# Performance work log

Hardware: AMD Instinct MI355X
Metric: run time of the kernel (lower is better)

Reference implementation:

```python
import jax, jax.numpy as jnp
import numpy as np


def setup_inputs() -> dict:
    key = jax.random.key(0)
    k1, k2, k3 = jax.random.split(key, 3)
    B, C, H, W = 8, 256, 128, 128
    G, P = 1024, 1024
    sample_map = jax.random.normal(k1, (B, C, H, W), dtype=jnp.float32)
    sample_pts = jax.random.uniform(k2, (G, P, 2), dtype=jnp.float32)
    batch_ids = jax.random.randint(k3, (G,), 0, B, dtype=jnp.int64)
    return {"sample_map": sample_map, "sample_pts": sample_pts, "batch_ids": batch_ids}


def reference(sample_map, sample_pts, batch_ids):
    # Faithful to MapSampler2d: per-group batch gather + F.grid_sample
    # (bilinear, padding_mode='zeros', align_corners=False on pts mapped to [-1,1]).
    B, C, H, W = sample_map.shape
    bid = batch_ids.astype(jnp.int32)

    g = 2.0 * sample_pts - 1.0                      # [G,P,2] in [-1,1]
    # align_corners=False unnormalization
    x = (g[..., 0] + 1.0) * (W * 0.5) - 0.5          # [G,P]
    y = (g[..., 1] + 1.0) * (H * 0.5) - 0.5

    x0f = jnp.floor(x)
    y0f = jnp.floor(y)
    wx = x - x0f                                     # [G,P]
    wy = y - y0f
    x0 = x0f.astype(jnp.int32)
    y0 = y0f.astype(jnp.int32)

    map_hwc = jnp.transpose(sample_map, (0, 2, 3, 1))  # [B,H,W,C]

    def gather(yi, xi):
        # zeros padding: out-of-bounds corners contribute 0
        valid = (yi >= 0) & (yi < H) & (xi >= 0) & (xi < W)
        yc = jnp.clip(yi, 0, H - 1)
        xc = jnp.clip(xi, 0, W - 1)
        v = map_hwc[bid[:, None], yc, xc]            # [G,P,C]
        return v * valid[..., None].astype(v.dtype)

    v00 = gather(y0, x0)
    v01 = gather(y0, x0 + 1)
    v10 = gather(y0 + 1, x0)
    v11 = gather(y0 + 1, x0 + 1)

    wx_ = wx[..., None]
    wy_ = wy[..., None]
    out = (v00 * (1.0 - wx_) * (1.0 - wy_)
           + v01 * wx_ * (1.0 - wy_)
           + v10 * (1.0 - wx_) * wy_
           + v11 * wx_ * wy_)                        # [G,P,C]
    return out
```

## Files before the change

### kernel.cpp

```cpp
#include <hip/hip_runtime.h>

#define Bv 8
#define Cv 256
#define Hv 128
#define Wv 128
#define HWv (Hv * Wv)
#define Gv 1024
#define Pv 1024
#define NBLK (256 * Gv)
#define SLOTS (NBLK / 8)

typedef __attribute__((ext_vector_type(4))) _Float16 half4;
typedef __attribute__((ext_vector_type(4))) float f32x4;

#define MAP_OFF_BYTES 8192

__global__ __launch_bounds__(256) void transpose_h_k(const float* __restrict__ in,
                                                     _Float16* __restrict__ out) {
    __shared__ float tile[64][33];
    int b  = blockIdx.z;
    int c0 = blockIdx.y * 64;
    int s0 = blockIdx.x * 32;
    int lin = threadIdx.x;
    int tx  = lin & 31;
    int ty  = lin >> 5;

    const float* ip = in + ((size_t)(b * Cv + c0 + ty)) * HWv + s0 + tx;
#pragma unroll
    for (int i = 0; i < 64; i += 8)
        tile[ty + i][tx] = ip[(size_t)i * HWv];
    __syncthreads();

    int cp = lin & 31;
    int r8 = lin >> 5;
#pragma unroll
    for (int it = 0; it < 4; ++it) {
        int r = r8 + it * 8;
        union { _Float16 h[2]; unsigned u; } pk;
        pk.h[0] = (_Float16)tile[2 * cp + 0][r];
        pk.h[1] = (_Float16)tile[2 * cp + 1][r];
        unsigned* dst = (unsigned*)(out + ((size_t)b * HWv + s0 + r) * Cv + c0);
        dst[cp] = pk.u;
    }
}

__global__ __launch_bounds__(1024) void prep_k(const int* __restrict__ bids,
                                               int* __restrict__ meta) {
    __shared__ int hist[8], base[8];
    int t = threadIdx.x;
    if (t < 8) hist[t] = 0;
    __syncthreads();
    int b = bids[t] & 7;
    int rank = atomicAdd(&hist[b], 1);
    __syncthreads();
    if (t == 0) {
        int acc = 0;
#pragma unroll
        for (int j = 0; j < 8; ++j) { base[j] = acc; acc += hist[j]; }
        int pl = 0, pe = 0;
#pragma unroll
        for (int j = 0; j < 8; ++j) {
            int W = hist[j] * 256;
            meta[1024 + j] = hist[j];
            meta[1032 + j] = base[j];
            meta[1040 + j] = W;
            meta[1048 + j] = pl;
            meta[1056 + j] = pe;
            pl += max(0, SLOTS - W);
            pe += max(0, W - SLOTS);
        }
    }
    __syncthreads();
    meta[base[b] + rank] = t;
}

__global__ __launch_bounds__(256) void sample_xcd_k(const _Float16* __restrict__ map,
                                                    const float* __restrict__ pts,
                                                    const int* __restrict__ meta,
                                                    float* __restrict__ out) {
    const int* perm = meta;
    const int* cnt  = meta + 1024;
    const int* off  = meta + 1032;
    const int* Wq   = meta + 1040;
    const int* PL   = meta + 1048;
    const int* PE   = meta + 1056;

    int bid = blockIdx.x;
    int k = bid & 7;
    int s = bid >> 3;

    int j, i;
    int Wk = Wq[k];
    if (s < Wk) {
        j = k; i = s;
    } else {
        int r = PL[k] + (s - Wk);
        j = 0;
#pragma unroll
        for (int q = 1; q < 8; ++q) j += (r >= PE[q]) ? 1 : 0;
        i = SLOTS + (r - PE[j]);
    }

    int half_items = cnt[j] << 7;
    int h  = (i >= half_items) ? 1 : 0;
    int rr = i - h * half_items;
    int gi = rr >> 7, chunk = rr & 127;
    int g  = perm[off[j] + gi];

    int t    = threadIdx.x;
    int wv   = t >> 6;
    int lane = t & 63;
    int hl   = lane & 31;
    int which = lane >> 5;
    int pt = (g << 10) + (chunk << 3) + (wv << 1) + which;

    float px = pts[2 * (size_t)pt + 0];
    float py = pts[2 * (size_t)pt + 1];

    float x = (float)Wv * px - 0.5f;
    float y = (float)Hv * py - 0.5f;
    float x0f = floorf(x), y0f = floorf(y);
    float wx = x - x0f, wy = y - y0f;
    int x0 = (int)x0f, y0 = (int)y0f;
    int x1 = x0 + 1,   y1 = y0 + 1;

    bool vx0 = (unsigned)x0 < (unsigned)Wv;
    bool vx1 = (unsigned)x1 < (unsigned)Wv;
    bool vy0 = (unsigned)y0 < (unsigned)Hv;
    bool vy1 = (unsigned)y1 < (unsigned)Hv;
    int xc0 = min(max(x0, 0), Wv - 1);
    int xc1 = min(max(x1, 0), Wv - 1);
    int yc0 = min(max(y0, 0), Hv - 1);
    int yc1 = min(max(y1, 0), Hv - 1);

    float w00 = (1.0f - wx) * (1.0f - wy) * ((vx0 & vy0) ? 1.0f : 0.0f);
    float w01 = wx * (1.0f - wy)          * ((vx1 & vy0) ? 1.0f : 0.0f);
    float w10 = (1.0f - wx) * wy          * ((vx0 & vy1) ? 1.0f : 0.0f);
    float w11 = wx * wy                   * ((vx1 & vy1) ? 1.0f : 0.0f);

    size_t bbase = (size_t)j * HWv * Cv;
    size_t o00 = bbase + ((size_t)yc0 * Wv + xc0) * Cv;
    size_t o01 = bbase + ((size_t)yc0 * Wv + xc1) * Cv;
    size_t o10 = bbase + ((size_t)yc1 * Wv + xc0) * Cv;
    size_t o11 = bbase + ((size_t)yc1 * Wv + xc1) * Cv;

    int c0 = (h << 7) + (hl << 2);

    half4 v00 = *(const half4*)(map + o00 + c0);
    half4 v01 = *(const half4*)(map + o01 + c0);
    half4 v10 = *(const half4*)(map + o10 + c0);
    half4 v11 = *(const half4*)(map + o11 + c0);

    f32x4 rr2;
    rr2.x = (float)v00.x * w00 + (float)v01.x * w01 + (float)v10.x * w10 + (float)v11.x * w11;
    rr2.y = (float)v00.y * w00 + (float)v01.y * w01 + (float)v10.y * w10 + (float)v11.y * w11;
    rr2.z = (float)v00.z * w00 + (float)v01.z * w01 + (float)v10.z * w10 + (float)v11.z * w11;
    rr2.w = (float)v00.w * w00 + (float)v01.w * w01 + (float)v10.w * w10 + (float)v11.w * w11;

    __builtin_nontemporal_store(rr2, (f32x4*)(out + (size_t)pt * Cv + c0));
}

__global__ __launch_bounds__(256) void sample_nchw_k(const float* __restrict__ map,
                                                     const float* __restrict__ pts,
                                                     const int* __restrict__ bids,
                                                     float* __restrict__ out) {
    int t    = blockIdx.x * 256 + threadIdx.x;
    int pt   = t >> 6;
    int lane = t & 63;

    int g = pt >> 10;
    float px = pts[2 * (size_t)pt + 0];
    float py = pts[2 * (size_t)pt + 1];
    int b = bids[g];
    float x = (float)Wv * px - 0.5f;
    float y = (float)Hv * py - 0.5f;
    float x0f = floorf(x), y0f = floorf(y);
    float wx = x - x0f, wy = y - y0f;
    int x0 = (int)x0f, y0 = (int)y0f;
    int x1 = x0 + 1,   y1 = y0 + 1;
    bool vx0 = (unsigned)x0 < (unsigned)Wv;
    bool vx1 = (unsigned)x1 < (unsigned)Wv;
    bool vy0 = (unsigned)y0 < (unsigned)Hv;
    bool vy1 = (unsigned)y1 < (unsigned)Hv;
    int xc0 = min(max(x0, 0), Wv - 1);
    int xc1 = min(max(x1, 0), Wv - 1);
    int yc0 = min(max(y0, 0), Hv - 1);
    int yc1 = min(max(y1, 0), Hv - 1);
    float w00 = (1.0f - wx) * (1.0f - wy) * ((vx0 & vy0) ? 1.0f : 0.0f);
    float w01 = wx * (1.0f - wy)          * ((vx1 & vy0) ? 1.0f : 0.0f);
    float w10 = (1.0f - wx) * wy          * ((vx0 & vy1) ? 1.0f : 0.0f);
    float w11 = wx * wy                   * ((vx1 & vy1) ? 1.0f : 0.0f);

    int c = lane * 4;
    const float* base = map + ((size_t)b * Cv + c) * HWv;
    size_t s00 = (size_t)yc0 * Wv + xc0;
    size_t s01 = (size_t)yc0 * Wv + xc1;
    size_t s10 = (size_t)yc1 * Wv + xc0;
    size_t s11 = (size_t)yc1 * Wv + xc1;

    f32x4 r;
#pragma unroll
    for (int jj = 0; jj < 4; ++jj) {
        const float* ch = base + (size_t)jj * HWv;
        r[jj] = ch[s00] * w00 + ch[s01] * w01 + ch[s10] * w10 + ch[s11] * w11;
    }
    *((f32x4*)(out + (size_t)pt * Cv) + lane) = r;
}

extern "C" void kernel_launch(void* const* d_in, const int* in_sizes, int n_in,
                              void* d_out, int out_size, void* d_ws, size_t ws_size,
                              hipStream_t stream) {
    const float* map  = (const float*)d_in[0];
    const float* pts  = (const float*)d_in[1];
    const int*   bids = (const int*)d_in[2];
    float*       out  = (float*)d_out;

    size_t need = MAP_OFF_BYTES + (size_t)Bv * HWv * Cv * sizeof(_Float16);
    int npts = Gv * Pv;

    if (ws_size >= need) {
        int*      meta = (int*)d_ws;
        _Float16* nhwc = (_Float16*)((char*)d_ws + MAP_OFF_BYTES);

        prep_k<<<1, 1024, 0, stream>>>(bids, meta);
        transpose_h_k<<<dim3(HWv / 32, Cv / 64, Bv), 256, 0, stream>>>(map, nhwc);
        sample_xcd_k<<<NBLK, 256, 0, stream>>>(nhwc, pts, meta, out);
    } else {
        int nblocks = npts * 64 / 256;
        sample_nchw_k<<<nblocks, 256, 0, stream>>>(map, pts, bids, out);
    }
}
```

Baseline: 284.6 us.

## Fuse prep into transpose kernel and sample two points per thread

Merges the batch-histogram prep kernel into the transpose launch as an extra z-slice, removing one kernel launch. The transpose now writes 16-byte packed fp16 vectors instead of 4-byte pairs. The sampling kernel handles two points per thread with half as many blocks and uses 32-bit offsets. It also reorders the block-to-slot mapping so spill-over work is scheduled first. This cuts block count and launch overhead and raises memory-level parallelism per thread, at the cost of more registers.

```diff
diff --git a/kernel.cpp b/kernel.cpp
--- a/kernel.cpp
+++ b/kernel.cpp
@@ -7,16 +7,58 @@
 #define HWv (Hv * Wv)
 #define Gv 1024
 #define Pv 1024
-#define NBLK (256 * Gv)
+#define NBLK (128 * Gv)
 #define SLOTS (NBLK / 8)
 
 typedef __attribute__((ext_vector_type(4))) _Float16 half4;
 typedef __attribute__((ext_vector_type(4))) float f32x4;
+typedef __attribute__((ext_vector_type(4))) unsigned u32x4;
 
 #define MAP_OFF_BYTES 8192
 
-__global__ __launch_bounds__(256) void transpose_h_k(const float* __restrict__ in,
-                                                     _Float16* __restrict__ out) {
+__global__ __launch_bounds__(256) void transpose_prep_k(const float* __restrict__ in,
+                                                        _Float16* __restrict__ out,
+                                                        const int* __restrict__ bids,
+                                                        int* __restrict__ meta) {
+    if (blockIdx.z == 8) {
+        if (blockIdx.x != 0 || blockIdx.y != 0) return;
+        __shared__ int hist[8], base[8];
+        int t = threadIdx.x;
+        if (t < 8) hist[t] = 0;
+        __syncthreads();
+        int rk[4], bb[4];
+#pragma unroll
+        for (int it = 0; it < 4; ++it) {
+            int g = t + it * 256;
+            int b = bids[g] & 7;
+            bb[it] = b;
+            rk[it] = atomicAdd(&hist[b], 1);
+        }
+        __syncthreads();
+        if (t == 0) {
+            int acc = 0;
+#pragma unroll
+            for (int j = 0; j < 8; ++j) { base[j] = acc; acc += hist[j]; }
+            int pl = 0, pe = 0;
+#pragma unroll
+            for (int j = 0; j < 8; ++j) {
+                int W = hist[j] * 128;
+                meta[1024 + j] = hist[j];
+                meta[1032 + j] = base[j];
+                meta[1040 + j] = W;
+                meta[1048 + j] = pl;
+                meta[1056 + j] = pe;
+                pl += max(0, SLOTS - W);
+                pe += max(0, W - SLOTS);
+            }
+        }
+        __syncthreads();
+#pragma unroll
+        for (int it = 0; it < 4; ++it)
+            meta[base[bb[it]] + rk[it]] = t + it * 256;
+        return;
+    }
+
     __shared__ float tile[64][33];
     int b  = blockIdx.z;
     int c0 = blockIdx.y * 64;
@@ -31,89 +73,19 @@
         tile[ty + i][tx] = ip[(size_t)i * HWv];
     __syncthreads();
 
-    int cp = lin & 31;
-    int r8 = lin >> 5;
-#pragma unroll
-    for (int it = 0; it < 4; ++it) {
-        int r = r8 + it * 8;
-        union { _Float16 h[2]; unsigned u; } pk;
-        pk.h[0] = (_Float16)tile[2 * cp + 0][r];
-        pk.h[1] = (_Float16)tile[2 * cp + 1][r];
-        unsigned* dst = (unsigned*)(out + ((size_t)b * HWv + s0 + r) * Cv + c0);
-        dst[cp] = pk.u;
-    }
-}
-
-__global__ __launch_bounds__(1024) void prep_k(const int* __restrict__ bids,
-                                               int* __restrict__ meta) {
-    __shared__ int hist[8], base[8];
-    int t = threadIdx.x;
-    if (t < 8) hist[t] = 0;
-    __syncthreads();
-    int b = bids[t] & 7;
-    int rank = atomicAdd(&hist[b], 1);
-    __syncthreads();
-    if (t == 0) {
-        int acc = 0;
-#pragma unroll
-        for (int j = 0; j < 8; ++j) { base[j] = acc; acc += hist[j]; }
-        int pl = 0, pe = 0;
-#pragma unroll
-        for (int j = 0; j < 8; ++j) {
-            int W = hist[j] * 256;
-            meta[1024 + j] = hist[j];
-            meta[1032 + j] = base[j];
-            meta[1040 + j] = W;
-            meta[1048 + j] = pl;
-            meta[1056 + j] = pe;
-            pl += max(0, SLOTS - W);
-            pe += max(0, W - SLOTS);
-        }
-    }
-    __syncthreads();
-    meta[base[b] + rank] = t;
-}
-
-__global__ __launch_bounds__(256) void sample_xcd_k(const _Float16* __restrict__ map,
-                                                    const float* __restrict__ pts,
-                                                    const int* __restrict__ meta,
-                                                    float* __restrict__ out) {
-    const int* perm = meta;
-    const int* cnt  = meta + 1024;
-    const int* off  = meta + 1032;
-    const int* Wq   = meta + 1040;
-    const int* PL   = meta + 1048;
-    const int* PE   = meta + 1056;
-
-    int bid = blockIdx.x;
-    int k = bid & 7;
-    int s = bid >> 3;
-
-    int j, i;
-    int Wk = Wq[k];
-    if (s < Wk) {
-        j = k; i = s;
-    } else {
-        int r = PL[k] + (s - Wk);
-        j = 0;
-#pragma unroll
-        for (int q = 1; q < 8; ++q) j += (r >= PE[q]) ? 1 : 0;
-        i = SLOTS + (r - PE[j]);
-    }
-
-    int half_items = cnt[j] << 7;
-    int h  = (i >= half_items) ? 1 : 0;
-    int rr = i - h * half_items;
-    int gi = rr >> 7, chunk = rr & 127;
-    int g  = perm[off[j] + gi];
-
-    int t    = threadIdx.x;
-    int wv   = t >> 6;
-    int lane = t & 63;
-    int hl   = lane & 31;
-    int which = lane >> 5;
-    int pt = (g << 10) + (chunk << 3) + (wv << 1) + which;
-
+    int r = lin >> 3;
+    int q = lin & 7;
+    union { _Float16 h[8]; u32x4 v; } pk;
+#pragma unroll
+    for (int k = 0; k < 8; ++k)
+        pk.h[k] = (_Float16)tile[8 * q + k][r];
+    u32x4* dst = (u32x4*)(out + ((size_t)b * HWv + s0 + r) * Cv + c0 + 8 * q);
+    *dst = pk.v;
+}
+
+__device__ __forceinline__ void point_setup_i(const float* __restrict__ pts, int pt, int bbase,
+                                              int& o00, int& o01, int& o10, int& o11,
+                                              float& w00, float& w01, float& w10, float& w11) {
     float px = pts[2 * (size_t)pt + 0];
     float py = pts[2 * (size_t)pt + 1];
 
@@ -133,31 +105,88 @@
     int yc0 = min(max(y0, 0), Hv - 1);
     int yc1 = min(max(y1, 0), Hv - 1);
 
-    float w00 = (1.0f - wx) * (1.0f - wy) * ((vx0 & vy0) ? 1.0f : 0.0f);
-    float w01 = wx * (1.0f - wy)          * ((vx1 & vy0) ? 1.0f : 0.0f);
-    float w10 = (1.0f - wx) * wy          * ((vx0 & vy1) ? 1.0f : 0.0f);
-    float w11 = wx * wy                   * ((vx1 & vy1) ? 1.0f : 0.0f);
-
-    size_t bbase = (size_t)j * HWv * Cv;
-    size_t o00 = bbase + ((size_t)yc0 * Wv + xc0) * Cv;
-    size_t o01 = bbase + ((size_t)yc0 * Wv + xc1) * Cv;
-    size_t o10 = bbase + ((size_t)yc1 * Wv + xc0) * Cv;
-    size_t o11 = bbase + ((size_t)yc1 * Wv + xc1) * Cv;
+    w00 = (1.0f - wx) * (1.0f - wy) * ((vx0 & vy0) ? 1.0f : 0.0f);
+    w01 = wx * (1.0f - wy)          * ((vx1 & vy0) ? 1.0f : 0.0f);
+    w10 = (1.0f - wx) * wy          * ((vx0 & vy1) ? 1.0f : 0.0f);
+    w11 = wx * wy                   * ((vx1 & vy1) ? 1.0f : 0.0f);
+
+    o00 = bbase + (yc0 * Wv + xc0) * Cv;
+    o01 = bbase + (yc0 * Wv + xc1) * Cv;
+    o10 = bbase + (yc1 * Wv + xc0) * Cv;
+    o11 = bbase + (yc1 * Wv + xc1) * Cv;
+}
+
+__global__ __launch_bounds__(256) void sample_xcd_k(const _Float16* __restrict__ map,
+                                                    const float* __restrict__ pts,
+                                                    const int* __restrict__ meta,
+                                                    float* __restrict__ out) {
+    const int* perm = meta;
+    const int* off  = meta + 1032;
+    const int* Wq   = meta + 1040;
+    const int* PL   = meta + 1048;
+    const int* PE   = meta + 1056;
+
+    int bid = blockIdx.x;
+    int k = bid & 7;
+    int s = bid >> 3;
+
+    int Wk = Wq[k];
+    int Lk = max(0, SLOTS - Wk);
+    int j, i;
+    if (s < Lk) {
+        int r = PL[k] + s;
+        j = 0;
+#pragma unroll
+        for (int q = 1; q < 8; ++q) j += (r >= PE[q]) ? 1 : 0;
+        i = SLOTS + (r - PE[j]);
+    } else {
+        j = k;
+        i = s - Lk;
+    }
+
+    int half_items = Wq[j] >> 1;
+    int h  = (i >= half_items) ? 1 : 0;
+    int r2 = i - h * half_items;
+    int gi = r2 >> 6, cp = r2 & 63;
+    int g  = perm[off[j] + gi];
+
+    int t    = threadIdx.x;
+    int wv   = t >> 6;
+    int lane = t & 63;
+    int hl   = lane & 31;
+    int which = lane >> 5;
+    int ptA = (g << 10) + (cp << 4) + (wv << 1) + which;
+    int ptB = ptA + 8;
+
+    int bbase = j * (HWv * Cv);
+    int a00, a01, a10, a11, b00, b01, b10, b11;
+    float wa00, wa01, wa10, wa11, wb00, wb01, wb10, wb11;
+    point_setup_i(pts, ptA, bbase, a00, a01, a10, a11, wa00, wa01, wa10, wa11);
+    point_setup_i(pts, ptB, bbase, b00, b01, b10, b11, wb00, wb01, wb10, wb11);
 
     int c0 = (h << 7) + (hl << 2);
 
-    half4 v00 = *(const half4*)(map + o00 + c0);
-    half4 v01 = *(const half4*)(map + o01 + c0);
-    half4 v10 = *(const half4*)(map + o10 + c0);
-    half4 v11 = *(const half4*)(map + o11 + c0);
-
-    f32x4 rr2;
-    rr2.x = (float)v00.x * w00 + (float)v01.x * w01 + (float)v10.x * w10 + (float)v11.x * w11;
-    rr2.y = (float)v00.y * w00 + (float)v01.y * w01 + (float)v10.y * w10 + (float)v11.y * w11;
-    rr2.z = (float)v00.z * w00 + (float)v01.z * w01 + (float)v10.z * w10 + (float)v11.z * w11;
-    rr2.w = (float)v00.w * w00 + (float)v01.w * w01 + (float)v10.w * w10 + (float)v11.w * w11;
-
-    __builtin_nontemporal_store(rr2, (f32x4*)(out + (size_t)pt * Cv + c0));
+    half4 va00 = *(const half4*)(map + a00 + c0);
+    half4 va01 = *(const half4*)(map + a01 + c0);
+    half4 va10 = *(const half4*)(map + a10 + c0);
+    half4 va11 = *(const half4*)(map + a11 + c0);
+    half4 vb00 = *(const half4*)(map + b00 + c0);
+    half4 vb01 = *(const half4*)(map + b01 + c0);
+    half4 vb10 = *(const half4*)(map + b10 + c0);
+    half4 vb11 = *(const half4*)(map + b11 + c0);
+
+    f32x4 rA, rB;
+    rA.x = (float)va00.x * wa00 + (float)va01.x * wa01 + (float)va10.x * wa10 + (float)va11.x * wa11;
+    rA.y = (float)va00.y * wa00 + (float)va01.y * wa01 + (float)va10.y * wa10 + (float)va11.y * wa11;
+    rA.z = (float)va00.z * wa00 + (float)va01.z * wa01 + (float)va10.z * wa10 + (float)va11.z * wa11;
+    rA.w = (float)va00.w * wa00 + (float)va01.w * wa01 + (float)va10.w * wa10 + (float)va11.w * wa11;
+    rB.x = (float)vb00.x * wb00 + (float)vb01.x * wb01 + (float)vb10.x * wb10 + (float)vb11.x * wb11;
+    rB.y = (float)vb00.y * wb00 + (float)vb01.y * wb01 + (float)vb10.y * wb10 + (float)vb11.y * wb11;
+    rB.z = (float)vb00.z * wb00 + (float)vb01.z * wb01 + (float)vb10.z * wb10 + (float)vb11.z * wb11;
+    rB.w = (float)vb00.w * wb00 + (float)vb01.w * wb01 + (float)vb10.w * wb10 + (float)vb11.w * wb11;
+
+    __builtin_nontemporal_store(rA, (f32x4*)(out + (size_t)ptA * Cv + c0));
+    __builtin_nontemporal_store(rB, (f32x4*)(out + (size_t)ptB * Cv + c0));
 }
 
 __global__ __launch_bounds__(256) void sample_nchw_k(const float* __restrict__ map,
@@ -222,8 +251,7 @@
         int*      meta = (int*)d_ws;
         _Float16* nhwc = (_Float16*)((char*)d_ws + MAP_OFF_BYTES);
 
-        prep_k<<<1, 1024, 0, stream>>>(bids, meta);
-        transpose_h_k<<<dim3(HWv / 32, Cv / 64, Bv), 256, 0, stream>>>(map, nhwc);
+        transpose_prep_k<<<dim3(HWv / 32, Cv / 64, Bv + 1), 256, 0, stream>>>(map, nhwc, bids, meta);
         sample_xcd_k<<<NBLK, 256, 0, stream>>>(nhwc, pts, meta, out);
     } else {
         int nblocks = npts * 64 / 256;
```

After: 252.3 us. 11.3% less time.
